# Optimization experiments

Hardware: AMD Instinct MI355X
Metric: run time of the kernel (lower is better)

The kernel has to match this reference:

```python
import jax, jax.numpy as jnp
import numpy as np

N_WIRES = 4
N_LAYERS = 4
N_PATCH = 14 * 14  # 196 2x2 patches of a 28x28 image


def _ry(state, theta, w):
    """Apply RY(theta) on wire w. state: (b, P, 2,2,2,2). theta: scalar or (b, P)."""
    ax = 2 + w
    s0 = jax.lax.slice_in_dim(state, 0, 1, axis=ax)
    s1 = jax.lax.slice_in_dim(state, 1, 2, axis=ax)
    c = jnp.cos(theta * 0.5)
    s = jnp.sin(theta * 0.5)
    if jnp.ndim(theta) > 0:  # per-(batch,patch) angles -> broadcast over wire axes
        c = c.reshape(c.shape + (1,) * N_WIRES)
        s = s.reshape(s.shape + (1,) * N_WIRES)
    return jnp.concatenate([c * s0 - s * s1, s * s0 + c * s1], axis=ax)


def _cx(state, ctrl, tgt):
    """Apply CNOT(ctrl, tgt): flip target axis on the ctrl=1 slice."""
    ca, ta = 2 + ctrl, 2 + tgt
    s0 = jax.lax.slice_in_dim(state, 0, 1, axis=ca)
    s1 = jnp.flip(jax.lax.slice_in_dim(state, 1, 2, axis=ca), axis=ta)
    return jnp.concatenate([s0, s1], axis=ca)


def setup_inputs() -> dict:
    key = jax.random.key(0)
    k1, k2, k3 = jax.random.split(key, 3)
    bsz = 8192
    x = jax.random.uniform(k1, (bsz, 784), dtype=jnp.float32)
    params = jax.random.normal(k2, (N_LAYERS, N_WIRES), dtype=jnp.float32)
    W = jax.random.normal(k3, (10, N_WIRES * N_PATCH), dtype=jnp.float32) * 0.03
    b = jnp.zeros((10,), dtype=jnp.float32)
    return {"x": x, "params": params, "W": W, "b": b}


def reference(x, params, W, b):
    bsz = x.shape[0]
    img = x.reshape(bsz, 28, 28)
    # 2x2 patches, row-major over (r, c), pixel order [r,c],[r,c+1],[r+1,c],[r+1,c+1]
    p = img.reshape(bsz, 14, 2, 14, 2).transpose(0, 1, 3, 2, 4).reshape(bsz, N_PATCH, 4)
    # |0000> state for every (batch, patch); all gates are real so real sim is exact
    state = jnp.zeros((bsz, N_PATCH, 2, 2, 2, 2), x.dtype).at[:, :, 0, 0, 0, 0].set(1.0)
    # encoder: RY(pixel) on each wire
    for w in range(N_WIRES):
        state = _ry(state, p[:, :, w], w)
    # ansatz: n_layers x (RY(param) per wire; CX(0,1); CX(2,3))
    for l in range(N_LAYERS):
        for w in range(N_WIRES):
            state = _ry(state, params[l, w], w)
        state = _cx(state, 0, 1)
        state = _cx(state, 2, 3)
    probs = state * state  # (b, P, 2,2,2,2)
    z = jnp.array([1.0, -1.0], x.dtype)  # PauliZ eigenvalues
    exp = jnp.stack([
        jnp.einsum('bpijkl,i->bp', probs, z),
        jnp.einsum('bpijkl,j->bp', probs, z),
        jnp.einsum('bpijkl,k->bp', probs, z),
        jnp.einsum('bpijkl,l->bp', probs, z),
    ], axis=-1)  # (b, P, 4), patch-major like torch.cat(patches, dim=1)
    feat = exp.reshape(bsz, N_PATCH * N_WIRES)
    logits = feat @ W.T + b
    return jax.nn.log_softmax(logits, axis=-1)
```

## Files before the change

kernel.cpp:

```cpp
#include <hip/hip_runtime.h>


#define RPB 4
#define NPIX 784
#define NPATCH 196

__global__ void build_U_kernel(const float* __restrict__ params, float* __restrict__ U) {
    int t = threadIdx.x;
    if (t >= 16) return;
    float st[16];
#pragma unroll
    for (int i = 0; i < 16; ++i) st[i] = (i == t) ? 1.0f : 0.0f;
#pragma unroll
    for (int l = 0; l < 4; ++l) {
#pragma unroll
        for (int w = 0; w < 4; ++w) {
            float ang = 0.5f * params[l * 4 + w];
            float c = cosf(ang), s = sinf(ang);
            const int m = 8 >> w;
#pragma unroll
            for (int idx = 0; idx < 16; ++idx) {
                if (idx & m) continue;
                float a0 = st[idx], a1 = st[idx | m];
                st[idx]     = c * a0 - s * a1;
                st[idx | m] = s * a0 + c * a1;
            }
        }
#pragma unroll
        for (int idx = 0; idx < 16; ++idx) {
            if ((idx & 8) && !(idx & 4)) { float tmp = st[idx]; st[idx] = st[idx | 4]; st[idx | 4] = tmp; }
        }
#pragma unroll
        for (int idx = 0; idx < 16; ++idx) {
            if ((idx & 2) && !(idx & 1)) { float tmp = st[idx]; st[idx] = st[idx | 1]; st[idx | 1] = tmp; }
        }
    }
#pragma unroll
    for (int s = 0; s < 16; ++s) U[s * 16 + t] = st[s];
}

__launch_bounds__(256, 8)
__global__ void quanv_kernel(const float* __restrict__ x,
                             const float* __restrict__ W,
                             const float* __restrict__ bias,
                             const float* __restrict__ U,
                             float* __restrict__ out,
                             int n_rows) {
    __shared__ __align__(16) float feat[RPB * NPIX];
    const int tid = threadIdx.x;
    const int row0 = blockIdx.x * RPB;

    for (int g = tid; g < RPB * NPATCH; g += 256) {
        int r = g / NPATCH;
        int P = g - r * NPATCH;
        int grow = row0 + r;
        float e0 = 0.f, e1 = 0.f, e2 = 0.f, e3 = 0.f;
        if (grow < n_rows) {
            int Pr = P / 14;
            int Pc = P - Pr * 14;
            const float* px = x + (size_t)grow * NPIX + Pr * 56 + Pc * 2;
            float2 t01 = *(const float2*)px;
            float2 t23 = *(const float2*)(px + 28);

            float c0 = __cosf(0.5f * t01.x), s0 = __sinf(0.5f * t01.x);
            float c1 = __cosf(0.5f * t01.y), s1 = __sinf(0.5f * t01.y);
            float c2 = __cosf(0.5f * t23.x), s2 = __sinf(0.5f * t23.x);
            float c3 = __cosf(0.5f * t23.y), s3 = __sinf(0.5f * t23.y);

            float pa[4] = { c0 * c1, c0 * s1, s0 * c1, s0 * s1 };
            float pb[4] = { c2 * c3, c2 * s3, s2 * c3, s2 * s3 };
            float v[16];
#pragma unroll
            for (int a = 0; a < 4; ++a)
#pragma unroll
                for (int b2 = 0; b2 < 4; ++b2)
                    v[a * 4 + b2] = pa[a] * pb[b2];

            float q[16];
#pragma unroll
            for (int s = 0; s < 16; ++s) {
                float acc = 0.f;
#pragma unroll
                for (int t2 = 0; t2 < 16; ++t2)
                    acc = fmaf(U[s * 16 + t2], v[t2], acc);
                q[s] = acc * acc;
            }

            float p0 = q[0] + q[1],   m0 = q[0] - q[1];
            float p1 = q[2] + q[3],   m1 = q[2] - q[3];
            float p2 = q[4] + q[5],   m2 = q[4] - q[5];
            float p3 = q[6] + q[7],   m3 = q[6] - q[7];
            float p4 = q[8] + q[9],   m4 = q[8] - q[9];
            float p5 = q[10] + q[11], m5 = q[10] - q[11];
            float p6 = q[12] + q[13], m6 = q[12] - q[13];
            float p7 = q[14] + q[15], m7 = q[14] - q[15];
            e3 = ((m0 + m1) + (m2 + m3)) + ((m4 + m5) + (m6 + m7));
            float P0 = p0 + p1, M0 = p0 - p1;
            float P1 = p2 + p3, M1 = p2 - p3;
            float P2 = p4 + p5, M2 = p4 - p5;
            float P3 = p6 + p7, M3 = p6 - p7;
            e2 = (M0 + M1) + (M2 + M3);
            e1 = (P0 - P1) + (P2 - P3);
            e0 = (P0 + P1) - (P2 + P3);
        }
        *(float4*)&feat[r * NPIX + 4 * P] = make_float4(e0, e1, e2, e3);
    }
    __syncthreads();

    const int wid = tid >> 6, lane = tid & 63;
    for (int r = wid; r < RPB; r += 4) {
        int grow = row0 + r;
        if (grow >= n_rows) break;
        float acc[10];
#pragma unroll
        for (int o = 0; o < 10; ++o) acc[o] = 0.f;
        const float* frow = &feat[r * NPIX];
        for (int k = lane; k < NPIX; k += 64) {
            float f = frow[k];
#pragma unroll
            for (int o = 0; o < 10; ++o)
                acc[o] = fmaf(f, W[o * NPIX + k], acc[o]);
        }
#pragma unroll
        for (int o = 0; o < 10; ++o) {
            acc[o] += __shfl_xor(acc[o], 32, 64);
            acc[o] += __shfl_xor(acc[o], 16, 64);
            acc[o] += __shfl_xor(acc[o], 8, 64);
            acc[o] += __shfl_xor(acc[o], 4, 64);
            acc[o] += __shfl_xor(acc[o], 2, 64);
            acc[o] += __shfl_xor(acc[o], 1, 64);
        }
        if (lane == 0) {
            float lg[10], mx = -1e30f;
#pragma unroll
            for (int o = 0; o < 10; ++o) { lg[o] = acc[o] + bias[o]; mx = fmaxf(mx, lg[o]); }
            float sum = 0.f;
#pragma unroll
            for (int o = 0; o < 10; ++o) sum += __expf(lg[o] - mx);
            float lse = mx + __logf(sum);
#pragma unroll
            for (int o = 0; o < 10; ++o) out[(size_t)grow * 10 + o] = lg[o] - lse;
        }
    }
}

extern "C" void kernel_launch(void* const* d_in, const int* in_sizes, int n_in,
                              void* d_out, int out_size, void* d_ws, size_t ws_size,
                              hipStream_t stream) {
    const float* x      = (const float*)d_in[0];
    const float* params = (const float*)d_in[1];
    const float* W      = (const float*)d_in[2];
    const float* b      = (const float*)d_in[3];
    float* out = (float*)d_out;
    float* U   = (float*)d_ws;

    int n_rows = in_sizes[0] / NPIX;

    hipLaunchKernelGGL(build_U_kernel, dim3(1), dim3(64), 0, stream, params, U);
    int nblocks = (n_rows + RPB - 1) / RPB;
    hipLaunchKernelGGL(quanv_kernel, dim3(nblocks), dim3(256), 0, stream,
                       x, W, b, U, out, n_rows);
}
```

Measured before the change: 98.79 us.

## Factor 16x16 circuit unitary into two 4x4 blocks and vectorize W loads

Exploits that the ansatz only entangles wires (0,1) and (2,3), so the 16x16 unitary factors into a tensor product of two 4x4 unitaries. Each patch now does two 4x4 matvecs instead of a 16x16 one, and the marginal expectations come straight from the two 4-element probability vectors. The 32 unitary entries are loaded into registers once per thread. The linear layer also reads features and W as float4, cutting load instructions, at the cost of more FMAs per iteration and fewer active lanes in that loop.

Result: faster. 87.51 us (-11.4%).

```diff
diff --git a/kernel.cpp b/kernel.cpp
--- a/kernel.cpp
+++ b/kernel.cpp
@@ -7,36 +7,34 @@
 
 __global__ void build_U_kernel(const float* __restrict__ params, float* __restrict__ U) {
     int t = threadIdx.x;
-    if (t >= 16) return;
-    float st[16];
+    if (t >= 8) return;
+    int pair = t >> 2;
+    int col  = t & 3;
+    float st[4];
 #pragma unroll
-    for (int i = 0; i < 16; ++i) st[i] = (i == t) ? 1.0f : 0.0f;
+    for (int i = 0; i < 4; ++i) st[i] = (i == col) ? 1.0f : 0.0f;
 #pragma unroll
     for (int l = 0; l < 4; ++l) {
+        float ah = 0.5f * params[l * 4 + pair * 2 + 0];
+        float al = 0.5f * params[l * 4 + pair * 2 + 1];
+        float ch = cosf(ah), sh = sinf(ah);
 #pragma unroll
-        for (int w = 0; w < 4; ++w) {
-            float ang = 0.5f * params[l * 4 + w];
-            float c = cosf(ang), s = sinf(ang);
-            const int m = 8 >> w;
+        for (int j = 0; j < 2; ++j) {
+            float u = st[j], w = st[j + 2];
+            st[j]     = ch * u - sh * w;
+            st[j + 2] = sh * u + ch * w;
+        }
+        float cl = cosf(al), sl = sinf(al);
 #pragma unroll
-            for (int idx = 0; idx < 16; ++idx) {
-                if (idx & m) continue;
-                float a0 = st[idx], a1 = st[idx | m];
-                st[idx]     = c * a0 - s * a1;
-                st[idx | m] = s * a0 + c * a1;
-            }
+        for (int j = 0; j < 4; j += 2) {
+            float u = st[j], w = st[j + 1];
+            st[j]     = cl * u - sl * w;
+            st[j + 1] = sl * u + cl * w;
         }
-#pragma unroll
-        for (int idx = 0; idx < 16; ++idx) {
-            if ((idx & 8) && !(idx & 4)) { float tmp = st[idx]; st[idx] = st[idx | 4]; st[idx | 4] = tmp; }
-        }
-#pragma unroll
-        for (int idx = 0; idx < 16; ++idx) {
-            if ((idx & 2) && !(idx & 1)) { float tmp = st[idx]; st[idx] = st[idx | 1]; st[idx | 1] = tmp; }
-        }
+        float tmp = st[2]; st[2] = st[3]; st[3] = tmp;
     }
 #pragma unroll
-    for (int s = 0; s < 16; ++s) U[s * 16 + t] = st[s];
+    for (int s = 0; s < 4; ++s) U[pair * 16 + s * 4 + col] = st[s];
 }
 
 __launch_bounds__(256, 8)
@@ -49,6 +47,10 @@
     __shared__ __align__(16) float feat[RPB * NPIX];
     const int tid = threadIdx.x;
     const int row0 = blockIdx.x * RPB;
+
+    float Ua[16], Ub[16];
+#pragma unroll
+    for (int i = 0; i < 16; ++i) { Ua[i] = U[i]; Ub[i] = U[16 + i]; }
 
     for (int g = tid; g < RPB * NPATCH; g += 256) {
         int r = g / NPATCH;
@@ -69,57 +71,44 @@
 
             float pa[4] = { c0 * c1, c0 * s1, s0 * c1, s0 * s1 };
             float pb[4] = { c2 * c3, c2 * s3, s2 * c3, s2 * s3 };
-            float v[16];
+
+            float qa[4], qb[4];
 #pragma unroll
-            for (int a = 0; a < 4; ++a)
-#pragma unroll
-                for (int b2 = 0; b2 < 4; ++b2)
-                    v[a * 4 + b2] = pa[a] * pb[b2];
-
-            float q[16];
-#pragma unroll
-            for (int s = 0; s < 16; ++s) {
-                float acc = 0.f;
-#pragma unroll
-                for (int t2 = 0; t2 < 16; ++t2)
-                    acc = fmaf(U[s * 16 + t2], v[t2], acc);
-                q[s] = acc * acc;
+            for (int s = 0; s < 4; ++s) {
+                float ya = fmaf(Ua[s * 4 + 3], pa[3],
+                           fmaf(Ua[s * 4 + 2], pa[2],
+                           fmaf(Ua[s * 4 + 1], pa[1], Ua[s * 4 + 0] * pa[0])));
+                float yb = fmaf(Ub[s * 4 + 3], pb[3],
+                           fmaf(Ub[s * 4 + 2], pb[2],
+                           fmaf(Ub[s * 4 + 1], pb[1], Ub[s * 4 + 0] * pb[0])));
+                qa[s] = ya * ya;
+                qb[s] = yb * yb;
             }
-
-            float p0 = q[0] + q[1],   m0 = q[0] - q[1];
-            float p1 = q[2] + q[3],   m1 = q[2] - q[3];
-            float p2 = q[4] + q[5],   m2 = q[4] - q[5];
-            float p3 = q[6] + q[7],   m3 = q[6] - q[7];
-            float p4 = q[8] + q[9],   m4 = q[8] - q[9];
-            float p5 = q[10] + q[11], m5 = q[10] - q[11];
-            float p6 = q[12] + q[13], m6 = q[12] - q[13];
-            float p7 = q[14] + q[15], m7 = q[14] - q[15];
-            e3 = ((m0 + m1) + (m2 + m3)) + ((m4 + m5) + (m6 + m7));
-            float P0 = p0 + p1, M0 = p0 - p1;
-            float P1 = p2 + p3, M1 = p2 - p3;
-            float P2 = p4 + p5, M2 = p4 - p5;
-            float P3 = p6 + p7, M3 = p6 - p7;
-            e2 = (M0 + M1) + (M2 + M3);
-            e1 = (P0 - P1) + (P2 - P3);
-            e0 = (P0 + P1) - (P2 + P3);
+            e0 = (qa[0] + qa[1]) - (qa[2] + qa[3]);
+            e1 = (qa[0] - qa[1]) + (qa[2] - qa[3]);
+            e2 = (qb[0] + qb[1]) - (qb[2] + qb[3]);
+            e3 = (qb[0] - qb[1]) + (qb[2] - qb[3]);
         }
         *(float4*)&feat[r * NPIX + 4 * P] = make_float4(e0, e1, e2, e3);
     }
     __syncthreads();
 
     const int wid = tid >> 6, lane = tid & 63;
+    const float4* W4 = (const float4*)W;
     for (int r = wid; r < RPB; r += 4) {
         int grow = row0 + r;
         if (grow >= n_rows) break;
         float acc[10];
 #pragma unroll
         for (int o = 0; o < 10; ++o) acc[o] = 0.f;
-        const float* frow = &feat[r * NPIX];
-        for (int k = lane; k < NPIX; k += 64) {
-            float f = frow[k];
+        const float4* frow4 = (const float4*)&feat[r * NPIX];
+        for (int k = lane; k < NPATCH; k += 64) {
+            float4 f = frow4[k];
 #pragma unroll
-            for (int o = 0; o < 10; ++o)
-                acc[o] = fmaf(f, W[o * NPIX + k], acc[o]);
+            for (int o = 0; o < 10; ++o) {
+                float4 w = W4[o * NPATCH + k];
+                acc[o] = fmaf(f.x, w.x, fmaf(f.y, w.y, fmaf(f.z, w.z, fmaf(f.w, w.w, acc[o]))));
+            }
         }
 #pragma unroll
         for (int o = 0; o < 10; ++o) {
```
